# Performance work log

Hardware: AMD Instinct MI355X
Metric: run time of the kernel (lower is better)

## Reference

```python
import jax, jax.numpy as jnp
import numpy as np

D_MODEL, N_LEVELS, N_HEADS, N_POINTS = 256, 4, 8, 4
SHAPES = [(100, 100), (50, 50), (25, 25), (13, 13)]  # (H, W) per level


def setup_inputs() -> dict:
    key = jax.random.key(0)
    ks = jax.random.split(key, 8)
    N = 2
    C = D_MODEL
    Len_in = sum(h * w for h, w in SHAPES)
    Lq = Len_in  # encoder self-attention
    query = jax.random.normal(ks[0], (N, Lq, C), jnp.float32)
    reference_points = jax.random.uniform(ks[1], (N, Lq, N_LEVELS, 2), dtype=jnp.float32)
    input_flatten = jax.random.normal(ks[2], (N, Len_in, C), jnp.float32)
    input_spatial_shapes = np.array(SHAPES, dtype=np.int64)
    areas = input_spatial_shapes[:, 0] * input_spatial_shapes[:, 1]
    input_level_start_index = np.concatenate([[0], np.cumsum(areas)[:-1]]).astype(np.int64)
    s = 1.0 / np.sqrt(C)
    Wv = jax.random.uniform(ks[3], (C, C), jnp.float32, -s, s)
    bv = jnp.zeros((C,), jnp.float32)
    # sampling_offsets: small random weight + the module's grid bias init
    Woff = jax.random.normal(ks[4], (N_HEADS * N_LEVELS * N_POINTS * 2, C), jnp.float32) * 0.01
    thetas = jnp.arange(N_HEADS, dtype=jnp.float32) * (2.0 * np.pi / N_HEADS)
    grid = jnp.stack([jnp.cos(thetas), jnp.sin(thetas)], -1)  # (M,2)
    grid = grid / jnp.max(jnp.abs(grid), axis=-1, keepdims=True)
    grid = jnp.tile(grid[:, None, None, :], (1, N_LEVELS, N_POINTS, 1))
    grid = grid * (jnp.arange(N_POINTS, dtype=jnp.float32) + 1.0)[None, None, :, None]
    boff = grid.reshape(-1)
    Wa = jax.random.normal(ks[5], (N_HEADS * N_LEVELS * N_POINTS, C), jnp.float32) * 0.02
    ba = jnp.zeros((N_HEADS * N_LEVELS * N_POINTS,), jnp.float32)
    Wo = jax.random.uniform(ks[6], (C, C), jnp.float32, -s, s)
    bo = jnp.zeros((C,), jnp.float32)
    return {
        'query': query, 'reference_points': reference_points, 'input_flatten': input_flatten,
        'input_spatial_shapes': input_spatial_shapes, 'input_level_start_index': input_level_start_index,
        'Wv': Wv, 'bv': bv, 'Woff': Woff, 'boff': boff, 'Wa': Wa, 'ba': ba, 'Wo': Wo, 'bo': bo,
    }


def _msda_forward(query, reference_points, input_flatten, shapes, starts,
                  Wv, bv, Woff, boff, Wa, ba, Wo, bo):
    N, Lq, C = query.shape
    M, L, P = N_HEADS, N_LEVELS, N_POINTS
    D = C // M
    value = (input_flatten @ Wv.T + bv).reshape(N, -1, M, D)  # (N, Len_in, M, D)
    off = (query @ Woff.T + boff).reshape(N, Lq, M, L, P, 2)
    attn = jax.nn.softmax((query @ Wa.T + ba).reshape(N, Lq, M, L * P), axis=-1)
    attn = attn.reshape(N, Lq, M, L, P)
    # offset_normalizer = (W_l, H_l)
    norm = jnp.asarray(shapes[:, ::-1].copy(), jnp.float32)  # (L, 2)
    loc = reference_points[:, :, None, :, None, :] + off / norm[None, None, None, :, None, :]
    grids = 2.0 * loc - 1.0  # (N, Lq, M, L, P, 2), grid_sample convention
    out = jnp.zeros((N, Lq, M, D), query.dtype)
    for l in range(L):
        H, W = int(shapes[l, 0]), int(shapes[l, 1])
        s0 = int(starts[l])
        v = value[:, s0:s0 + H * W]  # (N, H*W, M, D)
        # align_corners=False unnormalization
        gx = ((grids[:, :, :, l, :, 0] + 1.0) * W - 1.0) / 2.0  # (N, Lq, M, P)
        gy = ((grids[:, :, :, l, :, 1] + 1.0) * H - 1.0) / 2.0
        x0 = jnp.floor(gx); y0 = jnp.floor(gy)
        fx = gx - x0;       fy = gy - y0
        x0i = x0.astype(jnp.int32); y0i = y0.astype(jnp.int32)

        def gather(iy, ix):
            valid = (iy >= 0) & (iy < H) & (ix >= 0) & (ix < W)
            lin = jnp.clip(iy, 0, H - 1) * W + jnp.clip(ix, 0, W - 1)  # (N, Lq, M, P)
            lin2 = lin.transpose(0, 1, 3, 2).reshape(N, Lq * P, M)
            g = jnp.take_along_axis(v, lin2[..., None], axis=1)  # (N, Lq*P, M, D)
            g = g.reshape(N, Lq, P, M, D).transpose(0, 1, 3, 2, 4)  # (N, Lq, M, P, D)
            return g * valid[..., None]  # zero padding outside

        s00 = gather(y0i, x0i)
        s01 = gather(y0i, x0i + 1)
        s10 = gather(y0i + 1, x0i)
        s11 = gather(y0i + 1, x0i + 1)
        sampled = (s00 * ((1 - fy) * (1 - fx))[..., None] + s01 * ((1 - fy) * fx)[..., None]
                   + s10 * (fy * (1 - fx))[..., None] + s11 * (fy * fx)[..., None])
        out = out + jnp.einsum('nqmp,nqmpd->nqmd', attn[:, :, :, l], sampled)
    out = out.reshape(N, Lq, C)
    return out @ Wo.T + bo


def reference(query, reference_points, input_flatten, input_spatial_shapes, input_level_start_index,
              Wv, bv, Woff, boff, Wa, ba, Wo, bo):
    shapes = np.asarray(input_spatial_shapes)
    starts = np.asarray(input_level_start_index)
    return _msda_forward(query, reference_points, input_flatten, shapes, starts,
                         Wv, bv, Woff, boff, Wa, ba, Wo, bo)
```

## Files before the change

kernel.cpp:

```cpp
#include <hip/hip_runtime.h>
#include <math.h>

#define NB   2
#define LQ   13294
#define NROWS (NB*LQ)
#define CDIM 256

typedef unsigned short u16;
typedef unsigned int   u32;
typedef short bf16x8 __attribute__((ext_vector_type(8)));
typedef float f32x4  __attribute__((ext_vector_type(4)));
typedef float f32x2  __attribute__((ext_vector_type(2)));

struct alignas(8) U16x4 { u16 x, y, z, w; };

__device__ __forceinline__ u16 f2bf(float f) {
    u32 u = __builtin_bit_cast(u32, f);
    u += 0x7FFFu + ((u >> 16) & 1u);
    return (u16)(u >> 16);
}
__device__ __forceinline__ float bf2f(u16 h) {
    u32 u = ((u32)h) << 16;
    return __builtin_bit_cast(float, u);
}

__device__ __forceinline__ u32 cvtpk(float a, float b) {
    u32 d;
    asm("v_cvt_pk_bf16_f32 %0, %1, %2" : "=v"(d) : "v"(a), "v"(b));
    return d;
}

__device__ __forceinline__ void gload_lds16(const void* g, void* l) {
    __builtin_amdgcn_global_load_lds(
        (__attribute__((address_space(1))) void*)g,
        (__attribute__((address_space(3))) void*)l, 16, 0, 0);
}

__device__ __forceinline__ f32x2 bfpair(u32 u) {
    union { u32 w[2]; f32x2 v; } x;
    x.w[0] = u << 16;
    x.w[1] = u & 0xFFFF0000u;
    return x.v;
}

__device__ __forceinline__ void core_f32src(
    const float* __restrict__ A, const float* __restrict__ Bf, int M, int row0,
    u16* As, u16* Bs, f32x4 (&acc)[4][4]) {
    const int tid  = threadIdx.x;
    const int lane = tid & 63;
    const int wave = tid >> 6;
    const int ln16 = lane & 15;
    const int kq   = lane >> 4;
    const int wr   = (wave >> 1) * 64;
    const int wc   = (wave & 1) * 64;

    #pragma unroll
    for (int kt = 0; kt < 4; ++kt) {
        const int k0 = kt * 64;
        #pragma unroll
        for (int it = 0; it < 4; ++it) {
            int chunk = it * 256 + tid;
            int row = chunk >> 3;
            int ch  = chunk & 7;
            int dst = row * 64 + ((ch ^ (row & 7)) * 8);
            int gra = min(row0 + row, M - 1);
            const float* pa = A + (size_t)gra * 256 + k0 + ch * 8;
            float4 a0 = *(const float4*)pa;
            float4 a1 = *(const float4*)(pa + 4);
            uint4 ua;
            ua.x = cvtpk(a0.x, a0.y); ua.y = cvtpk(a0.z, a0.w);
            ua.z = cvtpk(a1.x, a1.y); ua.w = cvtpk(a1.z, a1.w);
            *(uint4*)&As[dst] = ua;
            const float* pb = Bf + (size_t)row * 256 + k0 + ch * 8;
            float4 b0 = *(const float4*)pb;
            float4 b1 = *(const float4*)(pb + 4);
            uint4 ub;
            ub.x = cvtpk(b0.x, b0.y); ub.y = cvtpk(b0.z, b0.w);
            ub.z = cvtpk(b1.x, b1.y); ub.w = cvtpk(b1.z, b1.w);
            *(uint4*)&Bs[dst] = ub;
        }
        __syncthreads();
        #pragma unroll
        for (int kf = 0; kf < 2; ++kf) {
            const int ck = kf * 4 + kq;
            bf16x8 a[4], b[4];
            #pragma unroll
            for (int i = 0; i < 4; ++i) {
                int r = wr + i * 16 + ln16;
                a[i] = *(const bf16x8*)&As[r * 64 + ((ck ^ (r & 7)) * 8)];
                int c = wc + i * 16 + ln16;
                b[i] = *(const bf16x8*)&Bs[c * 64 + ((ck ^ (c & 7)) * 8)];
            }
            #pragma unroll
            for (int i = 0; i < 4; ++i)
                #pragma unroll
                for (int j = 0; j < 4; ++j)
                    acc[i][j] = __builtin_amdgcn_mfma_f32_16x16x32_bf16(
                        a[i], b[j], acc[i][j], 0, 0, 0);
        }
        __syncthreads();
    }
}

__device__ __forceinline__ void core_mixed(
    const u16* __restrict__ A, const float* __restrict__ Bf, int M, int row0,
    u16* As, u16* Bs, f32x4 (&acc)[4][4]) {
    const int tid  = threadIdx.x;
    const int lane = tid & 63;
    const int wave = tid >> 6;
    const int ln16 = lane & 15;
    const int kq   = lane >> 4;
    const int wr   = (wave >> 1) * 64;
    const int wc   = (wave & 1) * 64;

    #pragma unroll
    for (int kt = 0; kt < 4; ++kt) {
        const int k0 = kt * 64;
        #pragma unroll
        for (int it = 0; it < 4; ++it) {
            int chunk = it * 256 + tid;
            int row = chunk >> 3;
            int ch  = chunk & 7;
            int chs = (ch ^ (row & 7)) * 8;
            int gra = min(row0 + row, M - 1);
            gload_lds16(A + (size_t)gra * 256 + k0 + chs, As + chunk * 8);
            const float* pb = Bf + (size_t)row * 256 + k0 + ch * 8;
            float4 b0 = *(const float4*)pb;
            float4 b1 = *(const float4*)(pb + 4);
            uint4 ub;
            ub.x = cvtpk(b0.x, b0.y); ub.y = cvtpk(b0.z, b0.w);
            ub.z = cvtpk(b1.x, b1.y); ub.w = cvtpk(b1.z, b1.w);
            *(uint4*)&Bs[row * 64 + chs] = ub;
        }
        __syncthreads();
        #pragma unroll
        for (int kf = 0; kf < 2; ++kf) {
            const int ck = kf * 4 + kq;
            bf16x8 a[4], b[4];
            #pragma unroll
            for (int i = 0; i < 4; ++i) {
                int r = wr + i * 16 + ln16;
                a[i] = *(const bf16x8*)&As[r * 64 + ((ck ^ (r & 7)) * 8)];
                int c = wc + i * 16 + ln16;
                b[i] = *(const bf16x8*)&Bs[c * 64 + ((ck ^ (c & 7)) * 8)];
            }
            #pragma unroll
            for (int i = 0; i < 4; ++i)
                #pragma unroll
                for (int j = 0; j < 4; ++j)
                    acc[i][j] = __builtin_amdgcn_mfma_f32_16x16x32_bf16(
                        a[i], b[j], acc[i][j], 0, 0, 0);
        }
        __syncthreads();
    }
}

__global__ __launch_bounds__(256, 3)
void gemm_front(const float* __restrict__ query, const float* __restrict__ inflat,
                const float* __restrict__ Wv, const float* __restrict__ Woff,
                const float* __restrict__ Wa, const float* __restrict__ bv,
                const float* __restrict__ boff, const float* __restrict__ ba,
                u16* __restrict__ value, float* __restrict__ offb,
                float* __restrict__ logit, int M) {
    __shared__ u16 As[128 * 64];
    __shared__ u16 Bs[128 * 64];
    const int s    = blockIdx.x;
    const int row0 = blockIdx.y * 128;
    const float* A  = (s < 2) ? inflat : query;
    const float* Bf = (s == 0) ? Wv
                    : (s == 1) ? Wv + 32768
                    : (s == 2) ? Woff
                    : (s == 3) ? Woff + 32768
                    : Wa;
    const float* bias = (s < 2) ? bv + s * 128
                      : (s < 4) ? boff + (s - 2) * 128
                      : ba;

    f32x4 acc[4][4] = {};
    core_f32src(A, Bf, M, row0, As, Bs, acc);

    const int lane = threadIdx.x & 63;
    const int wave = threadIdx.x >> 6;
    const int ln16 = lane & 15, kq = lane >> 4;
    const int wr = (wave >> 1) * 64, wc = (wave & 1) * 64;
    #pragma unroll
    for (int j = 0; j < 4; ++j) {
        int lc = wc + j * 16 + ln16;
        float bj = bias[lc];
        #pragma unroll
        for (int i = 0; i < 4; ++i) {
            #pragma unroll
            for (int r = 0; r < 4; ++r) {
                int gr = row0 + wr + i * 16 + kq * 4 + r;
                if (gr < M) {
                    float o = acc[i][j][r] + bj;
                    if (s < 2)
                        value[(size_t)gr * 256 + s * 128 + lc] = f2bf(o);
                    else if (s < 4)
                        offb[(size_t)gr * 256 + (s - 2) * 128 + lc] = o;
                    else
                        logit[(size_t)gr * 128 + lc] = o;
                }
            }
        }
    }
}

__global__ __launch_bounds__(256, 3)
void gemm_out(const u16* __restrict__ A, const float* __restrict__ Wo,
              const float* __restrict__ bias, float* __restrict__ C, int M) {
    __shared__ u16 As[128 * 64];
    __shared__ u16 Bs[128 * 64];
    const int s    = blockIdx.x;
    const int row0 = blockIdx.y * 128;
    const float* Bf = Wo + (size_t)s * 32768;

    f32x4 acc[4][4] = {};
    core_mixed(A, Bf, M, row0, As, Bs, acc);

    const int lane = threadIdx.x & 63;
    const int wave = threadIdx.x >> 6;
    const int ln16 = lane & 15, kq = lane >> 4;
    const int wr = (wave >> 1) * 64, wc = (wave & 1) * 64;
    #pragma unroll
    for (int j = 0; j < 4; ++j) {
        int gc = s * 128 + wc + j * 16 + ln16;
        float bj = bias[gc];
        #pragma unroll
        for (int i = 0; i < 4; ++i) {
            #pragma unroll
            for (int r = 0; r < 4; ++r) {
                int gr = row0 + wr + i * 16 + kq * 4 + r;
                if (gr < M) C[(size_t)gr * 256 + gc] = acc[i][j][r] + bj;
            }
        }
    }
}

__global__ __launch_bounds__(256)
void msda_sample(const u16* __restrict__ value,
                 const float* __restrict__ refpts,
                 const float* __restrict__ off,
                 const float* __restrict__ logits,
                 u16* __restrict__ tmp) {
    __shared__ float sAw[4][8][16];
    __shared__ int   sLin[4][8][17][4];
    __shared__ float sW[4][8][17][4];

    const int t  = threadIdx.x;
    const int qb = blockIdx.x * 4;

    if (t < 32) {
        const int qi = t >> 3, m = t & 7;
        const float* lg = logits + (size_t)(qb + qi) * 128 + m * 16;
        float e[16];
        float mx = -1e30f;
        #pragma unroll
        for (int i = 0; i < 16; ++i) { e[i] = lg[i]; mx = fmaxf(mx, e[i]); }
        float s = 0.f;
        #pragma unroll
        for (int i = 0; i < 16; ++i) { e[i] = __expf(e[i] - mx); s += e[i]; }
        const float inv = 1.f / s;
        #pragma unroll
        for (int i = 0; i < 16; ++i) sAw[qi][m][i] = e[i] * inv;
    }
    __syncthreads();

    #pragma unroll
    for (int j2 = 0; j2 < 2; ++j2) {
        const int job = t + j2 * 256;
        const int qi = job >> 7;
        const int m  = (job >> 4) & 7;
        const int p  = job & 15;
        const int l  = p >> 2, pp = p & 3;
        const int q  = qb + qi;
        const int n  = (q >= LQ) ? 1 : 0;

        const int W = (l == 0) ? 100 : (l == 1) ? 50 : (l == 2) ? 25 : 13;
        const int H = W;
        const int st = (l == 0) ? 0 : (l == 1) ? 10000 : (l == 2) ? 12500 : 13125;
        const float invW = (l == 0) ? 0.01f : (l == 1) ? 0.02f
                         : (l == 2) ? 0.04f : (1.f / 13.f);

        const float rx = refpts[(size_t)q * 8 + l * 2 + 0];
        const float ry = refpts[(size_t)q * 8 + l * 2 + 1];
        const float ox = off[(size_t)q * 256 + m * 32 + (l * 4 + pp) * 2 + 0];
        const float oy = off[(size_t)q * 256 + m * 32 + (l * 4 + pp) * 2 + 1];

        const float locx = rx + ox * invW;
        const float locy = ry + oy * invW;
        const float grx = 2.f * locx - 1.f;
        const float gry = 2.f * locy - 1.f;
        const float gx = ((grx + 1.f) * (float)W - 1.f) * 0.5f;
        const float gy = ((gry + 1.f) * (float)H - 1.f) * 0.5f;
        const float x0f = floorf(gx), y0f = floorf(gy);
        const float fx = gx - x0f, fy = gy - y0f;
        const int x0 = (int)x0f, y0 = (int)y0f;
        const int x1 = x0 + 1, y1 = y0 + 1;

        const int cx0 = min(max(x0, 0), W - 1);
        const int cx1 = min(max(x1, 0), W - 1);
        const int cy0 = min(max(y0, 0), H - 1);
        const int cy1 = min(max(y1, 0), H - 1);
        const bool vx0 = (x0 >= 0) & (x0 < W);
        const bool vx1 = (x1 >= 0) & (x1 < W);
        const bool vy0 = (y0 >= 0) & (y0 < H);
        const bool vy1 = (y1 >= 0) & (y1 < H);

        const float aw = sAw[qi][m][p];
        const int base = n * LQ + st;
        sLin[qi][m][p][0] = base + cy0 * W + cx0;
        sLin[qi][m][p][1] = base + cy0 * W + cx1;
        sLin[qi][m][p][2] = base + cy1 * W + cx0;
        sLin[qi][m][p][3] = base + cy1 * W + cx1;
        sW[qi][m][p][0] = (vy0 & vx0) ? aw * (1.f - fy) * (1.f - fx) : 0.f;
        sW[qi][m][p][1] = (vy0 & vx1) ? aw * (1.f - fy) * fx         : 0.f;
        sW[qi][m][p][2] = (vy1 & vx0) ? aw * fy * (1.f - fx)         : 0.f;
        sW[qi][m][p][3] = (vy1 & vx1) ? aw * fy * fx                 : 0.f;
    }
    __syncthreads();

    const int qi = t >> 6;
    const int m  = (t >> 3) & 7;
    const int hf = (t >> 2) & 1;
    const int e4 = t & 3;
    const int q  = qb + qi;
    const char* vb = (const char*)value;
    const u32 choff = (u32)(m * 64 + e4 * 16);

    f32x2 a2[4] = {{0.f, 0.f}, {0.f, 0.f}, {0.f, 0.f}, {0.f, 0.f}};
    #pragma unroll
    for (int pp = 0; pp < 8; ++pp) {
        const int p = hf * 8 + pp;
        int4   L  = *(const int4*)  &sLin[qi][m][p][0];
        float4 Wt = *(const float4*)&sW  [qi][m][p][0];
        uint4 r0 = *(const uint4*)(vb + ((u32)L.x * 512u + choff));
        uint4 r1 = *(const uint4*)(vb + ((u32)L.y * 512u + choff));
        uint4 r2 = *(const uint4*)(vb + ((u32)L.z * 512u + choff));
        uint4 r3 = *(const uint4*)(vb + ((u32)L.w * 512u + choff));
        {
            f32x2 w2 = {Wt.x, Wt.x};
            a2[0] += w2 * bfpair(r0.x); a2[1] += w2 * bfpair(r0.y);
            a2[2] += w2 * bfpair(r0.z); a2[3] += w2 * bfpair(r0.w);
        }
        {
            f32x2 w2 = {Wt.y, Wt.y};
            a2[0] += w2 * bfpair(r1.x); a2[1] += w2 * bfpair(r1.y);
            a2[2] += w2 * bfpair(r1.z); a2[3] += w2 * bfpair(r1.w);
        }
        {
            f32x2 w2 = {Wt.z, Wt.z};
            a2[0] += w2 * bfpair(r2.x); a2[1] += w2 * bfpair(r2.y);
            a2[2] += w2 * bfpair(r2.z); a2[3] += w2 * bfpair(r2.w);
        }
        {
            f32x2 w2 = {Wt.w, Wt.w};
            a2[0] += w2 * bfpair(r3.x); a2[1] += w2 * bfpair(r3.y);
            a2[2] += w2 * bfpair(r3.z); a2[3] += w2 * bfpair(r3.w);
        }
    }
    #pragma unroll
    for (int k = 0; k < 4; ++k) {
        a2[k].x += __shfl_xor(a2[k].x, 4);
        a2[k].y += __shfl_xor(a2[k].y, 4);
    }
    if (hf == 0) {
        uint4 o;
        o.x = (u32)f2bf(a2[0].x) | ((u32)f2bf(a2[0].y) << 16);
        o.y = (u32)f2bf(a2[1].x) | ((u32)f2bf(a2[1].y) << 16);
        o.z = (u32)f2bf(a2[2].x) | ((u32)f2bf(a2[2].y) << 16);
        o.w = (u32)f2bf(a2[3].x) | ((u32)f2bf(a2[3].y) << 16);
        *(uint4*)((char*)tmp + ((u32)q * 512u + choff)) = o;
    }
}

extern "C" void kernel_launch(void* const* d_in, const int* in_sizes, int n_in,
                              void* d_out, int out_size, void* d_ws, size_t ws_size,
                              hipStream_t stream) {
    const float* query  = (const float*)d_in[0];
    const float* refpts = (const float*)d_in[1];
    const float* inflat = (const float*)d_in[2];
    const float* Wv   = (const float*)d_in[5];
    const float* bv   = (const float*)d_in[6];
    const float* Woff = (const float*)d_in[7];
    const float* boff = (const float*)d_in[8];
    const float* Wa   = (const float*)d_in[9];
    const float* ba   = (const float*)d_in[10];
    const float* Wo   = (const float*)d_in[11];
    const float* bo   = (const float*)d_in[12];
    float* out = (float*)d_out;

    char* ws = (char*)d_ws;
    constexpr size_t SZ16 = (size_t)NROWS * 256 * 2;
    constexpr size_t SZ32 = (size_t)NROWS * 256 * 4;
    u16*   tmp   = (u16*)(ws);
    u16*   value = (u16*)(ws + 2 * SZ16);
    float* offb  = (float*)(ws + 3 * SZ16);
    float* logit = (float*)(ws + 3 * SZ16 + SZ32);

    const int RG = (NROWS + 127) / 128;

    gemm_front<<<dim3(5, RG), dim3(256), 0, stream>>>(
        query, inflat, Wv, Woff, Wa, bv, boff, ba, value, offb, logit, NROWS);

    hipLaunchKernelGGL(msda_sample, dim3(NROWS / 4), dim3(256), 0, stream,
                       value, refpts, offb, logit, tmp);

    gemm_out<<<dim3(2, RG), dim3(256), 0, stream>>>(
        tmp, Wo, bo, out, NROWS);
}
```

Before: 240.6 us.

## Store value head-major so bilinear x-neighbor pairs load as one contiguous span

The value projection is now written head-major: one slice of 32 channels per head, with rows contiguous at 64 bytes each, plus a zero padding row at the end. In the sampling kernel, 8 threads together load 128 contiguous bytes. That covers both horizontal neighbours x0 and x0+1 of a corner row, so each sampling point needs two gathers instead of four. Left-edge cases fold the weights so the loaded pair stays useful, and the padding row keeps right-edge reads in bounds. The cost is an extra write scattered over strided slices in the front GEMM epilogue and extra weight-selection logic.

```diff
diff --git a/kernel.cpp b/kernel.cpp
--- a/kernel.cpp
+++ b/kernel.cpp
@@ -5,6 +5,8 @@
 #define LQ   13294
 #define NROWS (NB*LQ)
 #define CDIM 256
+#define HSLICES (NROWS + 1)
+#define HS32 ((size_t)HSLICES * 32)
 
 typedef unsigned short u16;
 typedef unsigned int   u32;
@@ -18,10 +20,6 @@
     u32 u = __builtin_bit_cast(u32, f);
     u += 0x7FFFu + ((u >> 16) & 1u);
     return (u16)(u >> 16);
-}
-__device__ __forceinline__ float bf2f(u16 h) {
-    u32 u = ((u32)h) << 16;
-    return __builtin_bit_cast(float, u);
 }
 
 __device__ __forceinline__ u32 cvtpk(float a, float b) {
@@ -194,15 +192,20 @@
                 int gr = row0 + wr + i * 16 + kq * 4 + r;
                 if (gr < M) {
                     float o = acc[i][j][r] + bj;
-                    if (s < 2)
-                        value[(size_t)gr * 256 + s * 128 + lc] = f2bf(o);
-                    else if (s < 4)
+                    if (s < 2) {
+                        int c = s * 128 + lc;
+                        value[(size_t)(c >> 5) * HS32 + (size_t)gr * 32 + (c & 31)] = f2bf(o);
+                    } else if (s < 4)
                         offb[(size_t)gr * 256 + (s - 2) * 128 + lc] = o;
                     else
                         logit[(size_t)gr * 128 + lc] = o;
                 }
             }
         }
+    }
+    if (s == 0 && blockIdx.y == 0) {
+        int tt = threadIdx.x;
+        value[(size_t)(tt >> 5) * HS32 + (size_t)NROWS * 32 + (tt & 31)] = 0;
     }
 }
 
@@ -244,8 +247,8 @@
                  const float* __restrict__ logits,
                  u16* __restrict__ tmp) {
     __shared__ float sAw[4][8][16];
-    __shared__ int   sLin[4][8][17][4];
-    __shared__ float sW[4][8][17][4];
+    __shared__ int   sLin[4][8][16][2];
+    __shared__ float sW[4][8][16][4];
 
     const int t  = threadIdx.x;
     const int qb = blockIdx.x * 4;
@@ -309,68 +312,57 @@
 
         const float aw = sAw[qi][m][p];
         const int base = n * LQ + st;
+        const float w00 = (vy0 & vx0) ? aw * (1.f - fy) * (1.f - fx) : 0.f;
+        const float w01 = (vy0 & vx1) ? aw * (1.f - fy) * fx         : 0.f;
+        const float w10 = (vy1 & vx0) ? aw * fy * (1.f - fx)         : 0.f;
+        const float w11 = (vy1 & vx1) ? aw * fy * fx                 : 0.f;
+        const bool fold = (x0 < 0);
         sLin[qi][m][p][0] = base + cy0 * W + cx0;
-        sLin[qi][m][p][1] = base + cy0 * W + cx1;
-        sLin[qi][m][p][2] = base + cy1 * W + cx0;
-        sLin[qi][m][p][3] = base + cy1 * W + cx1;
-        sW[qi][m][p][0] = (vy0 & vx0) ? aw * (1.f - fy) * (1.f - fx) : 0.f;
-        sW[qi][m][p][1] = (vy0 & vx1) ? aw * (1.f - fy) * fx         : 0.f;
-        sW[qi][m][p][2] = (vy1 & vx0) ? aw * fy * (1.f - fx)         : 0.f;
-        sW[qi][m][p][3] = (vy1 & vx1) ? aw * fy * fx                 : 0.f;
+        sLin[qi][m][p][1] = base + cy1 * W + cx0;
+        sW[qi][m][p][0] = fold ? w01 : w00;
+        sW[qi][m][p][1] = fold ? 0.f : w01;
+        sW[qi][m][p][2] = fold ? w11 : w10;
+        sW[qi][m][p][3] = fold ? 0.f : w11;
     }
     __syncthreads();
 
     const int qi = t >> 6;
     const int m  = (t >> 3) & 7;
-    const int hf = (t >> 2) & 1;
-    const int e4 = t & 3;
+    const int e  = t & 7;
+    const int xh = e >> 2;
+    const int c4 = e & 3;
     const int q  = qb + qi;
-    const char* vb = (const char*)value;
-    const u32 choff = (u32)(m * 64 + e4 * 16);
+    const char* vb = (const char*)value + (size_t)m * (HS32 * 2);
+    const u32 eoff = (u32)e * 16u;
 
     f32x2 a2[4] = {{0.f, 0.f}, {0.f, 0.f}, {0.f, 0.f}, {0.f, 0.f}};
     #pragma unroll
-    for (int pp = 0; pp < 8; ++pp) {
-        const int p = hf * 8 + pp;
-        int4   L  = *(const int4*)  &sLin[qi][m][p][0];
-        float4 Wt = *(const float4*)&sW  [qi][m][p][0];
-        uint4 r0 = *(const uint4*)(vb + ((u32)L.x * 512u + choff));
-        uint4 r1 = *(const uint4*)(vb + ((u32)L.y * 512u + choff));
-        uint4 r2 = *(const uint4*)(vb + ((u32)L.z * 512u + choff));
-        uint4 r3 = *(const uint4*)(vb + ((u32)L.w * 512u + choff));
-        {
-            f32x2 w2 = {Wt.x, Wt.x};
-            a2[0] += w2 * bfpair(r0.x); a2[1] += w2 * bfpair(r0.y);
-            a2[2] += w2 * bfpair(r0.z); a2[3] += w2 * bfpair(r0.w);
-        }
-        {
-            f32x2 w2 = {Wt.y, Wt.y};
-            a2[0] += w2 * bfpair(r1.x); a2[1] += w2 * bfpair(r1.y);
-            a2[2] += w2 * bfpair(r1.z); a2[3] += w2 * bfpair(r1.w);
-        }
-        {
-            f32x2 w2 = {Wt.z, Wt.z};
-            a2[0] += w2 * bfpair(r2.x); a2[1] += w2 * bfpair(r2.y);
-            a2[2] += w2 * bfpair(r2.z); a2[3] += w2 * bfpair(r2.w);
-        }
-        {
-            f32x2 w2 = {Wt.w, Wt.w};
-            a2[0] += w2 * bfpair(r3.x); a2[1] += w2 * bfpair(r3.y);
-            a2[2] += w2 * bfpair(r3.z); a2[3] += w2 * bfpair(r3.w);
-        }
+    for (int p = 0; p < 16; ++p) {
+        int2   rb = *(const int2*)  &sLin[qi][m][p][0];
+        float4 w4 = *(const float4*)&sW  [qi][m][p][0];
+        uint4 r0 = *(const uint4*)(vb + ((u32)rb.x * 64u + eoff));
+        uint4 r1 = *(const uint4*)(vb + ((u32)rb.y * 64u + eoff));
+        const float wa = xh ? w4.y : w4.x;
+        const float wb_ = xh ? w4.w : w4.z;
+        f32x2 wa2 = {wa, wa};
+        f32x2 wb2 = {wb_, wb_};
+        a2[0] += wa2 * bfpair(r0.x); a2[1] += wa2 * bfpair(r0.y);
+        a2[2] += wa2 * bfpair(r0.z); a2[3] += wa2 * bfpair(r0.w);
+        a2[0] += wb2 * bfpair(r1.x); a2[1] += wb2 * bfpair(r1.y);
+        a2[2] += wb2 * bfpair(r1.z); a2[3] += wb2 * bfpair(r1.w);
     }
     #pragma unroll
     for (int k = 0; k < 4; ++k) {
         a2[k].x += __shfl_xor(a2[k].x, 4);
         a2[k].y += __shfl_xor(a2[k].y, 4);
     }
-    if (hf == 0) {
+    if (xh == 0) {
         uint4 o;
         o.x = (u32)f2bf(a2[0].x) | ((u32)f2bf(a2[0].y) << 16);
         o.y = (u32)f2bf(a2[1].x) | ((u32)f2bf(a2[1].y) << 16);
         o.z = (u32)f2bf(a2[2].x) | ((u32)f2bf(a2[2].y) << 16);
         o.w = (u32)f2bf(a2[3].x) | ((u32)f2bf(a2[3].y) << 16);
-        *(uint4*)((char*)tmp + ((u32)q * 512u + choff)) = o;
+        *(uint4*)((char*)tmp + ((u32)q * 512u + (u32)m * 64u + (u32)c4 * 16u)) = o;
     }
 }
 
@@ -391,12 +383,13 @@
     float* out = (float*)d_out;
 
     char* ws = (char*)d_ws;
-    constexpr size_t SZ16 = (size_t)NROWS * 256 * 2;
-    constexpr size_t SZ32 = (size_t)NROWS * 256 * 4;
+    constexpr size_t SZ16  = (size_t)NROWS * 256 * 2;
+    constexpr size_t SZVAL = ((size_t)HSLICES * 512 + 4095) & ~(size_t)4095;
+    constexpr size_t SZ32  = (size_t)NROWS * 256 * 4;
     u16*   tmp   = (u16*)(ws);
-    u16*   value = (u16*)(ws + 2 * SZ16);
-    float* offb  = (float*)(ws + 3 * SZ16);
-    float* logit = (float*)(ws + 3 * SZ16 + SZ32);
+    u16*   value = (u16*)(ws + SZ16);
+    float* offb  = (float*)(ws + SZ16 + SZVAL);
+    float* logit = (float*)(ws + SZ16 + SZVAL + SZ32);
 
     const int RG = (NROWS + 127) / 128;
 
```

Measured after the change: 223.3 us. 1.08x faster.
